# Kernel tuning notes

Hardware: AMD Instinct MI355X
Metric: run time of the kernel (lower is better)

Reference implementation:

```python
import jax, jax.numpy as jnp
import numpy as np

NUM_CLUSTERS = 512
EMBED_DIM = 256
BATCH = 65536
ALPHA = 0.05

def setup_inputs() -> dict:
    key = jax.random.key(0)
    k1, k2 = jax.random.split(key)
    embeddings = jax.random.normal(k1, (BATCH, EMBED_DIM), dtype=jnp.float32)
    # torch.randn centers drawn inside forward; materialized here for determinism
    centers = jax.random.normal(k2, (NUM_CLUSTERS, EMBED_DIM), dtype=jnp.float32)
    return {"embeddings": embeddings, "centers": centers}

def reference(embeddings, centers):
    # the broadcast difference, without the huge [N, K, D] intermediate).
    x_sq = jnp.sum(embeddings * embeddings, axis=1, keepdims=True)      # [N, 1]
    c_sq = jnp.sum(centers * centers, axis=1)[None, :]                  # [1, K]
    cross = embeddings @ centers.T                                      # [N, K]
    distances = jnp.sqrt(jnp.maximum(x_sq + c_sq - 2.0 * cross, 0.0))   # [N, K]
    cluster_assignments = jnp.argmin(distances, axis=1)                 # [N] int
    # gather distance to assigned (nearest) center
    cluster_loss = jnp.take_along_axis(
        distances, cluster_assignments[:, None], axis=1)[:, 0]          # [N]
    kmeans_loss = jnp.mean(cluster_loss)
    return kmeans_loss * ALPHA
```

## Files before the change

### kernel.cpp

```cpp
#include <hip/hip_runtime.h>
#include <hip/hip_bf16.h>

#define NROWS 65536
#define DIM   256
#define KC    512
#define ALPHA 0.05f

#define TROWS 16
#define NTILE 16
#define SLD   264

typedef __attribute__((ext_vector_type(8))) short bf16x8;
typedef __attribute__((ext_vector_type(4))) float f32x4;

static __device__ __forceinline__ unsigned short f2bf(float f) {
    union { __hip_bfloat16 h; unsigned short u; } c;
    c.h = __float2bfloat16(f);
    return c.u;
}
static __device__ __forceinline__ float bf2f(unsigned short u) {
    union { unsigned short u; __hip_bfloat16 h; } c;
    c.u = u;
    return __bfloat162float(c.h);
}

__global__ void prep_centers(const float* __restrict__ centers,
                             float* __restrict__ csqh,
                             uint4* __restrict__ cbf2,
                             float* __restrict__ out) {
    const int t = threadIdx.x;
    const int r = blockIdx.x * 8 + (t >> 5);
    const int e = t & 31;
    const float4* cv = reinterpret_cast<const float4*>(centers);
    float4 v0 = cv[r * 64 + e * 2];
    float4 v1 = cv[r * 64 + e * 2 + 1];
    float s = v0.x * v0.x + v0.y * v0.y + v0.z * v0.z + v0.w * v0.w
            + v1.x * v1.x + v1.y * v1.y + v1.z * v1.z + v1.w * v1.w;
    unsigned short o[8];
    o[0] = f2bf(v0.x); o[1] = f2bf(v0.y); o[2] = f2bf(v0.z); o[3] = f2bf(v0.w);
    o[4] = f2bf(v1.x); o[5] = f2bf(v1.y); o[6] = f2bf(v1.z); o[7] = f2bf(v1.w);
    const int cg = r >> 4, m = r & 15;
    const int kk = e >> 2, q = e & 3, l = q * 16 + m;
    cbf2[(cg * 8 + kk) * 64 + l] = *reinterpret_cast<uint4*>(o);
    #pragma unroll
    for (int off = 16; off; off >>= 1) s += __shfl_xor(s, off, 64);
    if (e == 0) csqh[r] = 0.5f * s;
    if (blockIdx.x == 0 && t == 0) out[0] = 0.f;
}

__global__ __launch_bounds__(512, 2) void kmeans_main(
    const float* __restrict__ emb,
    const uint4* __restrict__ cbf2,
    const float* __restrict__ csqh_g,
    float* __restrict__ out) {
    __shared__ unsigned short sA[2][TROWS * SLD];
    __shared__ float lmax[8][16];
    __shared__ float lx2[2][16];

    const int t = threadIdx.x;
    const int ww = t >> 6;
    const int lane = t & 63;
    const int m = lane & 15;
    const int q = lane >> 4;
    const int rr = t >> 5;
    const int e  = t & 31;

    const bf16x8* cb2 = reinterpret_cast<const bf16x8*>(cbf2);
    bf16x8 bfr[4][8];
    #pragma unroll
    for (int c = 0; c < 4; ++c)
        #pragma unroll
        for (int kk = 0; kk < 8; ++kk) {
            bf16x8 v = cb2[(((ww * 4 + c) * 8) + kk) * 64 + lane];
            asm volatile("" : "+v"(v));
            bfr[c][kk] = v;
        }
    float c2h[4];
    #pragma unroll
    for (int c = 0; c < 4; ++c) c2h[c] = csqh_g[(ww * 4 + c) * 16 + m];

    const float4* embv = reinterpret_cast<const float4*>(emb)
                       + (size_t)blockIdx.x * 256 * 64;

    auto A_LOAD = [&](int T, float4& l0, float4& l1) {
        l0 = embv[(T * 16 + rr) * 64 + e];
        l1 = embv[(T * 16 + rr) * 64 + 32 + e];
    };
    auto A_STAGE = [&](int T, float4 l0, float4 l1) {
        ushort4 o0, o1;
        o0.x = f2bf(l0.x); o0.y = f2bf(l0.y); o0.z = f2bf(l0.z); o0.w = f2bf(l0.w);
        o1.x = f2bf(l1.x); o1.y = f2bf(l1.y); o1.z = f2bf(l1.z); o1.w = f2bf(l1.w);
        *reinterpret_cast<ushort4*>(&sA[T & 1][rr * SLD + e * 4]) = o0;
        *reinterpret_cast<ushort4*>(&sA[T & 1][rr * SLD + 128 + e * 4]) = o1;
        float xa = bf2f(o0.x), xb = bf2f(o0.y), xc = bf2f(o0.z), xd = bf2f(o0.w);
        float xe = bf2f(o1.x), xf = bf2f(o1.y), xg = bf2f(o1.z), xh = bf2f(o1.w);
        float xs = xa*xa + xb*xb + xc*xc + xd*xd + xe*xe + xf*xf + xg*xg + xh*xh;
        xs += __shfl_xor(xs, 1, 64);  xs += __shfl_xor(xs, 2, 64);
        xs += __shfl_xor(xs, 4, 64);  xs += __shfl_xor(xs, 8, 64);
        xs += __shfl_xor(xs, 16, 64);
        if (e == 0) lx2[T & 1][rr] = xs;
    };

    float4 ldA0, ldA1, ldB0, ldB1;
    float dsum = 0.f;

    A_LOAD(0, ldA0, ldA1);
    A_LOAD(1, ldB0, ldB1);
    A_STAGE(0, ldA0, ldA1);

    #pragma unroll
    for (int tt = 0; tt < NTILE; ++tt) {
        if (tt + 1 < NTILE) {
            if ((tt & 1) == 0) A_STAGE(tt + 1, ldB0, ldB1);
            else               A_STAGE(tt + 1, ldA0, ldA1);
        }
        if (tt + 2 < NTILE) {
            if ((tt & 1) == 0) A_LOAD(tt + 2, ldA0, ldA1);
            else               A_LOAD(tt + 2, ldB0, ldB1);
        }
        asm volatile("s_waitcnt lgkmcnt(0)\n\ts_barrier" ::: "memory");

        f32x4 acc[4];
        #pragma unroll
        for (int c = 0; c < 4; ++c) {
            const float ci = -c2h[c];
            acc[c] = (f32x4){ci, ci, ci, ci};
        }
        #pragma unroll
        for (int kk = 0; kk < 8; ++kk) {
            bf16x8 a = *reinterpret_cast<const bf16x8*>(
                &sA[tt & 1][m * SLD + kk * 32 + q * 8]);
            #pragma unroll
            for (int c = 0; c < 4; ++c)
                acc[c] = __builtin_amdgcn_mfma_f32_16x16x32_bf16(
                    a, bfr[c][kk], acc[c], 0, 0, 0);
        }
        f32x4 mx;
        #pragma unroll
        for (int rg = 0; rg < 4; ++rg) {
            float v = fmaxf(fmaxf(acc[0][rg], acc[1][rg]),
                            fmaxf(acc[2][rg], acc[3][rg]));
            v = fmaxf(v, __shfl_xor(v, 1, 64));
            v = fmaxf(v, __shfl_xor(v, 2, 64));
            v = fmaxf(v, __shfl_xor(v, 4, 64));
            v = fmaxf(v, __shfl_xor(v, 8, 64));
            mx[rg] = v;
        }
        if (m == 0)
            *reinterpret_cast<float4*>(&lmax[ww][q * 4]) =
                (float4){mx[0], mx[1], mx[2], mx[3]};

        asm volatile("s_waitcnt lgkmcnt(0)\n\ts_barrier" ::: "memory");

        if (t < 16) {
            float M = lmax[0][t];
            #pragma unroll
            for (int j = 1; j < 8; ++j) M = fmaxf(M, lmax[j][t]);
            dsum += sqrtf(fmaxf(lx2[tt & 1][t] - 2.f * M, 0.f));
        }
    }

    if (t < 16) {
        dsum += __shfl_xor(dsum, 1, 64);
        dsum += __shfl_xor(dsum, 2, 64);
        dsum += __shfl_xor(dsum, 4, 64);
        dsum += __shfl_xor(dsum, 8, 64);
        if (t == 0) atomicAdd(out, dsum * (ALPHA / (float)NROWS));
    }
}

extern "C" void kernel_launch(void* const* d_in, const int* in_sizes, int n_in,
                              void* d_out, int out_size, void* d_ws, size_t ws_size,
                              hipStream_t stream) {
    const float* emb     = (const float*)d_in[0];
    const float* centers = (const float*)d_in[1];
    float* out = (float*)d_out;

    float* csqh = (float*)d_ws;
    uint4* cbf2 = (uint4*)((char*)d_ws + 2048);

    prep_centers<<<dim3(KC / 8), dim3(256), 0, stream>>>(centers, csqh, cbf2, out);
    kmeans_main<<<dim3(NROWS / 256), dim3(512), 0, stream>>>(emb, cbf2, csqh, out);
}
```

Before: 114.8 us.

## Drop per-tile second barrier, defer row-min reduction, deepen global prefetch

```diff
diff --git a/kernel.cpp b/kernel.cpp
--- a/kernel.cpp
+++ b/kernel.cpp
@@ -54,8 +54,9 @@
     const float* __restrict__ csqh_g,
     float* __restrict__ out) {
     __shared__ unsigned short sA[2][TROWS * SLD];
-    __shared__ float lmax[8][16];
-    __shared__ float lx2[2][16];
+    __shared__ float lmax[NTILE][8][16];
+    __shared__ float lx2[NTILE][16];
+    __shared__ float bsum[8];
 
     const int t = threadIdx.x;
     const int ww = t >> 6;
@@ -82,11 +83,14 @@
     const float4* embv = reinterpret_cast<const float4*>(emb)
                        + (size_t)blockIdx.x * 256 * 64;
 
-    auto A_LOAD = [&](int T, float4& l0, float4& l1) {
-        l0 = embv[(T * 16 + rr) * 64 + e];
-        l1 = embv[(T * 16 + rr) * 64 + 32 + e];
+    float4 pf[3][2];
+
+    auto A_LOAD = [&](int T) {
+        pf[T % 3][0] = embv[(T * 16 + rr) * 64 + e];
+        pf[T % 3][1] = embv[(T * 16 + rr) * 64 + 32 + e];
     };
-    auto A_STAGE = [&](int T, float4 l0, float4 l1) {
+    auto A_STAGE = [&](int T) {
+        float4 l0 = pf[T % 3][0], l1 = pf[T % 3][1];
         ushort4 o0, o1;
         o0.x = f2bf(l0.x); o0.y = f2bf(l0.y); o0.z = f2bf(l0.z); o0.w = f2bf(l0.w);
         o1.x = f2bf(l1.x); o1.y = f2bf(l1.y); o1.z = f2bf(l1.z); o1.w = f2bf(l1.w);
@@ -98,27 +102,19 @@
         xs += __shfl_xor(xs, 1, 64);  xs += __shfl_xor(xs, 2, 64);
         xs += __shfl_xor(xs, 4, 64);  xs += __shfl_xor(xs, 8, 64);
         xs += __shfl_xor(xs, 16, 64);
-        if (e == 0) lx2[T & 1][rr] = xs;
+        if (e == 0) lx2[T][rr] = xs;
     };
 
-    float4 ldA0, ldA1, ldB0, ldB1;
-    float dsum = 0.f;
-
-    A_LOAD(0, ldA0, ldA1);
-    A_LOAD(1, ldB0, ldB1);
-    A_STAGE(0, ldA0, ldA1);
+    A_LOAD(0);
+    A_LOAD(1);
+    A_LOAD(2);
+    A_STAGE(0);
 
     #pragma unroll
     for (int tt = 0; tt < NTILE; ++tt) {
-        if (tt + 1 < NTILE) {
-            if ((tt & 1) == 0) A_STAGE(tt + 1, ldB0, ldB1);
-            else               A_STAGE(tt + 1, ldA0, ldA1);
-        }
-        if (tt + 2 < NTILE) {
-            if ((tt & 1) == 0) A_LOAD(tt + 2, ldA0, ldA1);
-            else               A_LOAD(tt + 2, ldB0, ldB1);
-        }
         asm volatile("s_waitcnt lgkmcnt(0)\n\ts_barrier" ::: "memory");
+        if (tt + 1 < NTILE) A_STAGE(tt + 1);
+        if (tt + 3 < NTILE) A_LOAD(tt + 3);
 
         f32x4 acc[4];
         #pragma unroll
@@ -135,7 +131,6 @@
                 acc[c] = __builtin_amdgcn_mfma_f32_16x16x32_bf16(
                     a, bfr[c][kk], acc[c], 0, 0, 0);
         }
-        f32x4 mx;
         #pragma unroll
         for (int rg = 0; rg < 4; ++rg) {
             float v = fmaxf(fmaxf(acc[0][rg], acc[1][rg]),
@@ -144,28 +139,31 @@
             v = fmaxf(v, __shfl_xor(v, 2, 64));
             v = fmaxf(v, __shfl_xor(v, 4, 64));
             v = fmaxf(v, __shfl_xor(v, 8, 64));
-            mx[rg] = v;
-        }
-        if (m == 0)
-            *reinterpret_cast<float4*>(&lmax[ww][q * 4]) =
-                (float4){mx[0], mx[1], mx[2], mx[3]};
-
-        asm volatile("s_waitcnt lgkmcnt(0)\n\ts_barrier" ::: "memory");
-
-        if (t < 16) {
-            float M = lmax[0][t];
-            #pragma unroll
-            for (int j = 1; j < 8; ++j) M = fmaxf(M, lmax[j][t]);
-            dsum += sqrtf(fmaxf(lx2[tt & 1][t] - 2.f * M, 0.f));
+            if (m == 0) lmax[tt][ww][q * 4 + rg] = v;
         }
     }
+    asm volatile("s_waitcnt lgkmcnt(0)\n\ts_barrier" ::: "memory");
 
-    if (t < 16) {
-        dsum += __shfl_xor(dsum, 1, 64);
-        dsum += __shfl_xor(dsum, 2, 64);
-        dsum += __shfl_xor(dsum, 4, 64);
-        dsum += __shfl_xor(dsum, 8, 64);
-        if (t == 0) atomicAdd(out, dsum * (ALPHA / (float)NROWS));
+    float dsum = 0.f;
+    if (t < 256) {
+        const int tl = t >> 4, r = t & 15;
+        float M = lmax[tl][0][r];
+        #pragma unroll
+        for (int j = 1; j < 8; ++j) M = fmaxf(M, lmax[tl][j][r]);
+        dsum = sqrtf(fmaxf(lx2[tl][r] - 2.f * M, 0.f));
+    }
+    dsum += __shfl_xor(dsum, 1, 64);
+    dsum += __shfl_xor(dsum, 2, 64);
+    dsum += __shfl_xor(dsum, 4, 64);
+    dsum += __shfl_xor(dsum, 8, 64);
+    dsum += __shfl_xor(dsum, 16, 64);
+    dsum += __shfl_xor(dsum, 32, 64);
+    if (lane == 0) bsum[ww] = dsum;
+    asm volatile("s_waitcnt lgkmcnt(0)\n\ts_barrier" ::: "memory");
+    if (t == 0) {
+        float s = bsum[0] + bsum[1] + bsum[2] + bsum[3]
+                + bsum[4] + bsum[5] + bsum[6] + bsum[7];
+        atomicAdd(out, s * (ALPHA / (float)NROWS));
     }
 }
 
```

After: 116.7 us. No clear change (+1.6%).
